# Kernel optimization log

Measured on AMD Instinct MI355X. Metric: run time of the kernel, lower is better.

The kernel has to match this reference:

```python
import jax, jax.numpy as jnp
import numpy as np

N, E, B, D, H, L = 50000, 800000, 16, 64, 128, 2


def _lin(h, w, b):
    return h @ w + b


def _scatter_mean(v, idx, n):
    s = jax.ops.segment_sum(v, idx, num_segments=n)
    c = jax.ops.segment_sum(jnp.ones((v.shape[0],), v.dtype), idx, num_segments=n)
    return s / jnp.maximum(c, 1.0)[:, None]


def setup_inputs() -> dict:
    key = jax.random.key(0)
    ks = iter(jax.random.split(key, 40))

    def p(*shape):
        return jax.random.normal(next(ks), shape, dtype=jnp.float32) * 0.05

    inp = {
        "x": jax.random.normal(next(ks), (N, D), dtype=jnp.float32),
        "edge_attr": jax.random.normal(next(ks), (E, D), dtype=jnp.float32),
        "u": jax.random.normal(next(ks), (B, D), dtype=jnp.float32),
        "e_w1": p(L, 4 * D, H), "e_b1": p(L, H),
        "e_w2": p(L, H, H), "e_b2": p(L, H),
        "e_w3": p(L, H, D), "e_b3": p(L, D),
        "n1_w1": p(L, 2 * D, H), "n1_b1": p(L, H),
        "n1_w2": p(L, H, H), "n1_b2": p(L, H),
        "n2_w1": p(L, D + H + D, H), "n2_b1": p(L, H),
        "n2_w2": p(L, H, D), "n2_b2": p(L, D),
        "g_w1": p(L, 3 * D, H), "g_b1": p(L, H),
        "g_w2": p(L, H, D), "g_b2": p(L, D),
        "edge_index": jax.random.randint(next(ks), (2, E), 0, N, dtype=jnp.int32),
        "batch": jnp.sort(jax.random.randint(next(ks), (N,), 0, B, dtype=jnp.int32)),
    }
    return inp


def _forward(x, edge_attr, u, params, edge_index, batch):
    row, col = edge_index[0], edge_index[1]
    eb = batch[row]  # [E] graph id per edge
    x0, e0, u0 = x, edge_attr, u
    for l in range(L):
        (e_w1, e_b1, e_w2, e_b2, e_w3, e_b3,
         n1_w1, n1_b1, n1_w2, n1_b2,
         n2_w1, n2_b1, n2_w2, n2_b2,
         g_w1, g_b1, g_w2, g_b2) = [pm[l] for pm in params]
        # Edge model: [E, e+2n+u] -> MLP -> [E, D]
        h = jnp.concatenate([x[row], x[col], edge_attr, u[eb]], axis=1)
        h = jax.nn.relu(_lin(h, e_w1, e_b1))
        h = jax.nn.relu(_lin(h, e_w2, e_b2))
        edge_attr = _lin(h, e_w3, e_b3)
        # Node model: gather src node + edge, MLP1, scatter_mean onto dest, MLP2
        se = jnp.concatenate([x[row], edge_attr], axis=1)  # [E, 2D]
        se = _lin(jax.nn.relu(_lin(se, n1_w1, n1_b1)), n1_w2, n1_b2)
        agg = _scatter_mean(se, col, N)  # [N, H]
        xh = jnp.concatenate([x, agg, u[batch]], axis=1)
        x = _lin(jax.nn.relu(_lin(xh, n2_w1, n2_b1)), n2_w2, n2_b2)
        # Global model: per-graph means of updated nodes/edges
        e_agg = _scatter_mean(edge_attr, eb, B)
        n_agg = _scatter_mean(x, batch, B)
        uh = jnp.concatenate([u, n_agg, e_agg], axis=1)
        u = _lin(jax.nn.relu(_lin(uh, g_w1, g_b1)), g_w2, g_b2)
    return x + x0, edge_attr + e0, u + u0


def reference(x, edge_attr, u, e_w1, e_b1, e_w2, e_b2, e_w3, e_b3, n1_w1, n1_b1, n1_w2, n1_b2, n2_w1, n2_b1, n2_w2, n2_b2, g_w1, g_b1, g_w2, g_b2, edge_index, batch):
    params = (e_w1, e_b1, e_w2, e_b2, e_w3, e_b3,
              n1_w1, n1_b1, n1_w2, n1_b2,
              n2_w1, n2_b1, n2_w2, n2_b2,
              g_w1, g_b1, g_w2, g_b2)
    return _forward(x, edge_attr, u, params, edge_index, batch)
```

## Files before the change

### kernel.cpp

```cpp
#include <hip/hip_runtime.h>

#define N_NODES 50000
#define E_EDGES 800000
#define NG 16
#define DD 64
#define HH 128
#define NB_SCAN 49
#define EREP 32

typedef __attribute__((ext_vector_type(8))) __bf16 bf16x8;
typedef __attribute__((ext_vector_type(4))) float f32x4;
typedef unsigned int uint;
typedef unsigned short ushort;
typedef __attribute__((ext_vector_type(4))) uint uint4v;

#define MFMA16(a,b,c) __builtin_amdgcn_mfma_f32_16x16x32_bf16((a),(b),(c),0,0,0)

__device__ __forceinline__ ushort f2bf(float f){
  uint u = __builtin_bit_cast(uint, f);
  u += 0x7fffu + ((u >> 16) & 1u);
  return (ushort)(u >> 16);
}
__device__ __forceinline__ uint pk2(float a, float b){
  return (uint)f2bf(a) | ((uint)f2bf(b) << 16);
}
__device__ __forceinline__ float bflo(uint u){ return __builtin_bit_cast(float, u << 16); }
__device__ __forceinline__ float bfhi(uint u){ return __builtin_bit_cast(float, u & 0xffff0000u); }

__device__ __forceinline__ void bar(){
  asm volatile("s_waitcnt lgkmcnt(0)" ::: "memory");
  __builtin_amdgcn_s_barrier();
}
#define VMWAIT(n) asm volatile("s_waitcnt vmcnt(" #n ")" ::: "memory")

__device__ __forceinline__ void gload16(const void* g, void* l){
  __builtin_amdgcn_global_load_lds(
      (const __attribute__((address_space(1))) unsigned int*)g,
      (__attribute__((address_space(3))) unsigned int*)l, 16, 0, 0);
}

__device__ __forceinline__ bf16x8 ldfrag(const char* base, int row, int byteoff){
  uint4v v = *(const uint4v*)(base + row*256 + (byteoff ^ ((row & 7) << 4)));
  return __builtin_bit_cast(bf16x8, v);
}
__device__ __forceinline__ uint4v ld_chunk(const char* base, int row, int c16){
  return *(const uint4v*)(base + row*256 + ((c16*16) ^ ((row & 7) << 4)));
}
__device__ __forceinline__ void st_h(char* base, int row, int col, float v){
  *(ushort*)(base + row*256 + ((col*2) ^ ((row & 7) << 4))) = f2bf(v);
}
__device__ __forceinline__ void st_chunk(char* base, int row, int c16, uint4v v){
  *(uint4v*)(base + row*256 + ((c16*16) ^ ((row & 7) << 4))) = v;
}
__device__ __forceinline__ bf16x8 ldfrag128(const char* base, int row, int byteoff){
  uint4v v = *(const uint4v*)(base + row*128 + (byteoff ^ ((row & 7) << 4)));
  return __builtin_bit_cast(bf16x8, v);
}
__device__ __forceinline__ void st_chunk128(char* base, int row, int c16, uint4v v){
  *(uint4v*)(base + row*128 + ((c16*16) ^ ((row & 7) << 4))) = v;
}
__device__ __forceinline__ void pack16_128(char* dst, int r, int c16, const float* src){
  float4 lo = *(const float4*)src;
  float4 hi = *(const float4*)(src + 4);
  uint4v v; v.x = pk2(lo.x, lo.y); v.y = pk2(lo.z, lo.w);
  v.z = pk2(hi.x, hi.y); v.w = pk2(hi.z, hi.w);
  st_chunk128(dst, r, c16, v);
}

__device__ __forceinline__ void stage_b(char* sB, const ushort* wt,
                                        int Nout, int Ktot, int koff, int t, int stride){
  for (int task = t; task < Nout*16; task += stride){
    int n = task >> 4, c = task & 15;
    uint4v v = *(const uint4v*)(wt + (long)n*Ktot + koff + c*8);
    st_chunk(sB, n, c, v);
  }
}
template<int NT>
__device__ __forceinline__ void gemm_acc(const char* A, const char* B,
                                         int wv, int l15, int lhi, f32x4* acc){
  #pragma unroll
  for (int kt = 0; kt < 4; ++kt){
    bf16x8 a = ldfrag(A, wv*16 + l15, kt*64 + lhi*16);
    #pragma unroll
    for (int n = 0; n < NT; ++n){
      bf16x8 bb = ldfrag(B, n*16 + l15, kt*64 + lhi*16);
      acc[n] = MFMA16(a, bb, acc[n]);
    }
  }
}
template<int NT, bool RELU>
__device__ __forceinline__ void epi_lds(char* dst, const f32x4* acc, const float* bias,
                                        int wv, int l15, int lhi){
  #pragma unroll
  for (int n = 0; n < NT; ++n){
    float bv = bias[n*16 + l15];
    #pragma unroll
    for (int j = 0; j < 4; ++j){
      int r = wv*16 + lhi*4 + j;
      float v = acc[n][j] + bv;
      if (RELU) v = fmaxf(v, 0.f);
      st_h(dst, r, n*16 + l15, v);
    }
  }
}

__global__ void convert_x(const float* __restrict__ x, ushort* __restrict__ xbf){
  int i = blockIdx.x*256 + threadIdx.x;
  if (i < (N_NODES*DD)/8){
    float4 lo = *(const float4*)(x + (long)i*8);
    float4 hi = *(const float4*)(x + (long)i*8 + 4);
    uint4v v; v.x = pk2(lo.x, lo.y); v.y = pk2(lo.z, lo.w);
    v.z = pk2(hi.x, hi.y); v.w = pk2(hi.z, hi.w);
    *(uint4v*)(xbf + (long)i*8) = v;
  }
}

__global__ void pack_weights(const float* __restrict__ e1, const float* __restrict__ e2,
                             const float* __restrict__ e3, const float* __restrict__ n12,
                             const float* __restrict__ n21, const float* __restrict__ n22,
                             ushort* __restrict__ out){
  int idx = blockIdx.x * 256 + threadIdx.x;
  int l = idx / 114688, r = idx % 114688;
  const float* src; int K, N, off;
  if      (r <  32768){ src = e1;  K = 256; N = 128; off = 0; }
  else if (r <  49152){ src = e2;  K = 128; N = 128; off = 32768; }
  else if (r <  57344){ src = e3;  K = 128; N = 64;  off = 49152; }
  else if (r <  73728){ src = n12; K = 128; N = 128; off = 57344; }
  else if (r < 106496){ src = n21; K = 256; N = 128; off = 73728; }
  else                { src = n22; K = 128; N = 64;  off = 106496; }
  int q = r - off; int k = q / N; int n = q % N;
  out[(long)l*139264 + off + n*K + k] = f2bf(src[(long)l*K*N + q]);
}

__global__ void make_wc(const float* __restrict__ n1w1, const float* __restrict__ ew3,
                        const float* __restrict__ n1b1, const float* __restrict__ eb3,
                        ushort* __restrict__ packed, float* __restrict__ biasc){
  int l = blockIdx.x, t = threadIdx.x;
  const float* W1 = n1w1 + (long)l*128*128;
  const float* W3 = ew3 + (long)l*128*64;
  ushort* wc = packed + (long)l*139264 + 114688;
  for (int i = t; i < 8192; i += 256){
    int k = i >> 7, n = i & 127;
    wc[n*192 + k] = f2bf(W1[k*128 + n]);
  }
  for (int i = t; i < 16384; i += 256){
    int k2 = i >> 7, n = i & 127;
    float s = 0.f;
    for (int m = 0; m < 64; ++m) s += W3[k2*64 + m] * W1[(64 + m)*128 + n];
    wc[n*192 + 64 + k2] = f2bf(s);
  }
  if (t < 128){
    float s = n1b1[l*128 + t];
    for (int m = 0; m < 64; ++m) s += eb3[l*64 + m] * W1[(64 + m)*128 + t];
    biasc[l*128 + t] = s;
  }
}

__global__ void hist_kernel(const int* __restrict__ edge_index, const int* __restrict__ batch,
                            int* __restrict__ deg, float* __restrict__ cnt_eb){
  __shared__ float h[NG];
  int t = threadIdx.x;
  if (t < NG) h[t] = 0.f;
  __syncthreads();
  int e = blockIdx.x * 256 + t;
  if (e < E_EDGES){
    atomicAdd(deg + edge_index[E_EDGES + e], 1);
    atomicAdd(&h[batch[edge_index[e]]], 1.f);
  }
  __syncthreads();
  if (t < NG) atomicAdd(cnt_eb + t, h[t]);
}
__global__ void count_nodes_kernel(const int* __restrict__ batch, float* __restrict__ cnt_b){
  __shared__ float h[NG];
  int t = threadIdx.x;
  if (t < NG) h[t] = 0.f;
  __syncthreads();
  int n = blockIdx.x * 256 + t;
  if (n < N_NODES) atomicAdd(&h[batch[n]], 1.f);
  __syncthreads();
  if (t < NG) atomicAdd(cnt_b + t, h[t]);
}
__global__ void scan_a(const int* __restrict__ deg, int* __restrict__ bsum){
  __shared__ int red[1024];
  int i = blockIdx.x*1024 + threadIdx.x;
  red[threadIdx.x] = (i < N_NODES) ? deg[i] : 0;
  __syncthreads();
  for (int s = 512; s > 0; s >>= 1){
    if ((int)threadIdx.x < s) red[threadIdx.x] += red[threadIdx.x + s];
    __syncthreads();
  }
  if (threadIdx.x == 0) bsum[blockIdx.x] = red[0];
}
__global__ void scan_b(const int* __restrict__ bsum, int* __restrict__ bbase){
  if (threadIdx.x == 0){
    int run = 0;
    for (int b = 0; b < NB_SCAN; ++b){ int v = bsum[b]; bbase[b] = run; run += v; }
  }
}
__global__ void scan_c(const int* __restrict__ deg, const int* __restrict__ bbase,
                       int* __restrict__ off, int* __restrict__ cursor){
  __shared__ int sc[1024];
  int i = blockIdx.x*1024 + threadIdx.x;
  int v = (i < N_NODES) ? deg[i] : 0;
  sc[threadIdx.x] = v;
  __syncthreads();
  for (int d = 1; d < 1024; d <<= 1){
    int add = ((int)threadIdx.x >= d) ? sc[threadIdx.x - d] : 0;
    __syncthreads();
    sc[threadIdx.x] += add;
    __syncthreads();
  }
  if (i < N_NODES){
    int ex = sc[threadIdx.x] - v + bbase[blockIdx.x];
    off[i] = ex; cursor[i] = ex;
  }
}
__global__ void fill_kernel(const int* __restrict__ edge_index, int* __restrict__ cursor,
                            int* __restrict__ pos){
  int e = blockIdx.x*256 + threadIdx.x;
  if (e < E_EDGES){
    int c = edge_index[E_EDGES + e];
    pos[e] = atomicAdd(&cursor[c], 1);
  }
}

__global__ __launch_bounds__(256, 3) void k123_kernel(
    const ushort* __restrict__ xbf, const float* e_cur,
    const float* __restrict__ u_cur,
    const int* __restrict__ ei, const int* __restrict__ batch,
    const ushort* __restrict__ w1t, const ushort* __restrict__ w2t,
    const float* __restrict__ be1, const float* __restrict__ be2,
    ushort* h2g)
{
  __shared__ __align__(16) char lds[49152];
  __shared__ int sRow[128], sCol[128], sEb[128];
  char* A  = lds;
  char* B  = lds + 16384;
  char* OV = lds + 16384;
  const int t = threadIdx.x;
  const int wv = t >> 6, l15 = t & 15, lhi = (t >> 4) & 3;
  const int ebase = blockIdx.x * 128;

  if (t < 128){
    int r = ei[ebase + t];
    sRow[t] = r; sCol[t] = ei[E_EDGES + ebase + t]; sEb[t] = batch[r];
  }
  __syncthreads();

  f32x4 acc[2][8];
  #pragma unroll
  for (int m = 0; m < 2; ++m)
    #pragma unroll
    for (int n = 0; n < 8; ++n) acc[m][n] = f32x4{0,0,0,0};

  for (int c = 0; c < 4; ++c){
    #pragma unroll
    for (int it = 0; it < 4; ++it){
      int task = t + it*256, r = task >> 3, c16 = task & 7;
      if (c == 0)
        st_chunk128(A, r, c16, *(const uint4v*)(xbf + (long)sRow[r]*DD + c16*8));
      else if (c == 1)
        st_chunk128(A, r, c16, *(const uint4v*)(xbf + (long)sCol[r]*DD + c16*8));
      else if (c == 2)
        pack16_128(A, r, c16, e_cur + (long)(ebase + r)*DD + c16*8);
      else
        pack16_128(A, r, c16, u_cur + (long)sEb[r]*DD + c16*8);
    }
    #pragma unroll
    for (int it = 0; it < 4; ++it){
      int task = t + it*256, n = task >> 3, c16 = task & 7;
      st_chunk128(B, n, c16, *(const uint4v*)(w1t + (long)n*256 + c*64 + c16*8));
    }
    __syncthreads();
    #pragma unroll
    for (int kt = 0; kt < 2; ++kt){
      bf16x8 a0 = ldfrag128(A, wv*32 + l15,      kt*64 + lhi*16);
      bf16x8 a1 = ldfrag128(A, wv*32 + 16 + l15, kt*64 + lhi*16);
      #pragma unroll
      for (int n = 0; n < 8; ++n){
        bf16x8 bb = ldfrag128(B, n*16 + l15, kt*64 + lhi*16);
        acc[0][n] = MFMA16(a0, bb, acc[0][n]);
        acc[1][n] = MFMA16(a1, bb, acc[1][n]);
      }
    }
    __syncthreads();
  }
  #pragma unroll
  for (int m = 0; m < 2; ++m)
    #pragma unroll
    for (int n = 0; n < 8; ++n){
      int col = n*16 + l15;
      float bv = be1[col];
      #pragma unroll
      for (int j = 0; j < 4; ++j)
        st_h(OV, wv*32 + m*16 + lhi*4 + j, col, fmaxf(acc[m][n][j] + bv, 0.f));
    }
  __syncthreads();

  #pragma unroll
  for (int m = 0; m < 2; ++m)
    #pragma unroll
    for (int n = 0; n < 8; ++n) acc[m][n] = f32x4{0,0,0,0};
  for (int kc = 0; kc < 2; ++kc){
    #pragma unroll
    for (int it = 0; it < 4; ++it){
      int task = t + it*256, n = task >> 3, c16 = task & 7;
      st_chunk128(A, n, c16, *(const uint4v*)(w2t + (long)n*128 + kc*64 + c16*8));
    }
    __syncthreads();
    #pragma unroll
    for (int kt = 0; kt < 2; ++kt){
      bf16x8 a0 = ldfrag(OV, wv*32 + l15,      kc*128 + kt*64 + lhi*16);
      bf16x8 a1 = ldfrag(OV, wv*32 + 16 + l15, kc*128 + kt*64 + lhi*16);
      #pragma unroll
      for (int n = 0; n < 8; ++n){
        bf16x8 bb = ldfrag128(A, n*16 + l15, kt*64 + lhi*16);
        acc[0][n] = MFMA16(a0, bb, acc[0][n]);
        acc[1][n] = MFMA16(a1, bb, acc[1][n]);
      }
    }
    __syncthreads();
  }
  #pragma unroll
  for (int m = 0; m < 2; ++m)
    #pragma unroll
    for (int n = 0; n < 8; ++n){
      int col = n*16 + l15;
      float bv = be2[col];
      #pragma unroll
      for (int j = 0; j < 4; ++j)
        st_h(OV, wv*32 + m*16 + lhi*4 + j, col, fmaxf(acc[m][n][j] + bv, 0.f));
    }
  __syncthreads();
  #pragma unroll
  for (int it = 0; it < 8; ++it){
    int task = t + it*256, r = task >> 4, c16 = task & 15;
    *(uint4v*)(h2g + (long)(ebase + r)*HH + c16*8) = ld_chunk(OV, r, c16);
  }
}

template<bool CSR>
__global__ __launch_bounds__(256, 2) void k45_kernel(
    const ushort* __restrict__ xbf, const ushort* h2g,
    const int* __restrict__ ei, const int* __restrict__ batch,
    const int* __restrict__ pos_arr,
    const ushort* __restrict__ w3t, const ushort* __restrict__ wct,
    const ushort* __restrict__ w5t,
    const float* __restrict__ be3, const float* __restrict__ biasc,
    const float* __restrict__ bn12,
    float* e_outf, const float* __restrict__ e_resid,
    ushort* __restrict__ se_buf, float* __restrict__ agg_sum,
    float* __restrict__ e_agg_rep, int has_resid)
{
  __shared__ __align__(16) char lds[49152];
  __shared__ float sEagg[NG*DD];
  __shared__ int sRow[128];
  __shared__ int sDst[128];
  char* S0 = lds;
  char* S1 = lds + 16384;
  char* S2 = lds + 32768;
  char* OV = lds;
  const int t = threadIdx.x;
  const int wv = t >> 6, lane = t & 63, l15 = t & 15, lhi = (t >> 4) & 3;
  const int ebase = blockIdx.x * 128;

  auto GL = [&](const ushort* base, long stride, int koff, char* slot){
    #pragma unroll
    for (int it = 0; it < 4; ++it){
      int q = (wv*4 + it)*64 + lane;
      int r = q >> 3, cp = q & 7;
      gload16(base + (long)r*stride + koff + ((cp ^ (r & 7))*8),
              slot + (wv*4 + it)*1024);
    }
  };

  if (t < 128){
    int r = ei[ebase + t];
    sDst[t] = CSR ? pos_arr[ebase + t] : ei[E_EDGES + ebase + t];
    sRow[t] = r | (batch[r] << 16);
  }
  GL(wct, 192, 0, S1);
  GL(h2g + (long)ebase*HH, HH, 0, S2);
  bf16x8 b3[4][4];
  #pragma unroll
  for (int n = 0; n < 4; ++n)
    #pragma unroll
    for (int kk = 0; kk < 4; ++kk)
      b3[n][kk] = *(const bf16x8*)(w3t + (long)(n*16 + l15)*128 + kk*32 + lhi*8);
  for (int i = t; i < NG*DD; i += 256) sEagg[i] = 0.f;
  __syncthreads();

  #pragma unroll
  for (int it = 0; it < 4; ++it){
    int task = t + it*256, r = task >> 3, c16 = task & 7;
    st_chunk128(S0, r, c16,
        *(const uint4v*)(xbf + (long)(sRow[r] & 0xffff)*DD + c16*8));
  }
  __syncthreads();

  f32x4 acc4[2][8], acc3[2][4];
  #pragma unroll
  for (int m = 0; m < 2; ++m){
    #pragma unroll
    for (int n = 0; n < 8; ++n) acc4[m][n] = f32x4{0,0,0,0};
    #pragma unroll
    for (int n = 0; n < 4; ++n) acc3[m][n] = f32x4{0,0,0,0};
  }
  auto MM = [&](const char* A, const char* B){
    #pragma unroll
    for (int kt = 0; kt < 2; ++kt){
      bf16x8 a0 = ldfrag128(A, wv*32 + l15,      kt*64 + lhi*16);
      bf16x8 a1 = ldfrag128(A, wv*32 + 16 + l15, kt*64 + lhi*16);
      #pragma unroll
      for (int n = 0; n < 8; ++n){
        bf16x8 bb = ldfrag128(B, n*16 + l15, kt*64 + lhi*16);
        acc4[0][n] = MFMA16(a0, bb, acc4[0][n]);
        acc4[1][n] = MFMA16(a1, bb, acc4[1][n]);
      }
    }
  };
  auto MM3 = [&](const char* A, const char* B, int kkbase){
    #pragma unroll
    for (int kt = 0; kt < 2; ++kt){
      bf16x8 a0 = ldfrag128(A, wv*32 + l15,      kt*64 + lhi*16);
      bf16x8 a1 = ldfrag128(A, wv*32 + 16 + l15, kt*64 + lhi*16);
      #pragma unroll
      for (int n = 0; n < 8; ++n){
        bf16x8 bb = ldfrag128(B, n*16 + l15, kt*64 + lhi*16);
        acc4[0][n] = MFMA16(a0, bb, acc4[0][n]);
        acc4[1][n] = MFMA16(a1, bb, acc4[1][n]);
      }
      #pragma unroll
      for (int n = 0; n < 4; ++n){
        acc3[0][n] = MFMA16(a0, b3[n][kkbase + kt], acc3[0][n]);
        acc3[1][n] = MFMA16(a1, b3[n][kkbase + kt], acc3[1][n]);
      }
    }
  };

  MM(S0, S1);
  bar();
  GL(wct, 192, 64, S1);
  GL(h2g + (long)ebase*HH, HH, 64, S0);
  VMWAIT(4);
  __builtin_amdgcn_s_barrier();
  MM3(S2, S1, 0);
  bar();
  GL(wct, 192, 128, S1);
  GL(w5t, 128, 0, S2);
  VMWAIT(4);
  __builtin_amdgcn_s_barrier();
  MM3(S0, S1, 2);
  bar();
  #pragma unroll
  for (int m = 0; m < 2; ++m)
    #pragma unroll
    for (int n = 0; n < 8; ++n){
      int col = n*16 + l15;
      float bv = biasc[col];
      #pragma unroll
      for (int j = 0; j < 4; ++j)
        st_h(OV, wv*32 + m*16 + lhi*4 + j, col, fmaxf(acc4[m][n][j] + bv, 0.f));
    }
  VMWAIT(0);
  bar();
  f32x4 acc5[2][8];
  #pragma unroll
  for (int m = 0; m < 2; ++m)
    #pragma unroll
    for (int n = 0; n < 8; ++n) acc5[m][n] = f32x4{0,0,0,0};
  #pragma unroll
  for (int kt = 0; kt < 2; ++kt){
    bf16x8 a0 = ldfrag(OV, wv*32 + l15,      kt*64 + lhi*16);
    bf16x8 a1 = ldfrag(OV, wv*32 + 16 + l15, kt*64 + lhi*16);
    #pragma unroll
    for (int n = 0; n < 8; ++n){
      bf16x8 bb = ldfrag128(S2, n*16 + l15, kt*64 + lhi*16);
      acc5[0][n] = MFMA16(a0, bb, acc5[0][n]);
      acc5[1][n] = MFMA16(a1, bb, acc5[1][n]);
    }
  }
  bar();
  GL(w5t, 128, 64, S2);
  VMWAIT(0);
  __builtin_amdgcn_s_barrier();
  #pragma unroll
  for (int kt = 0; kt < 2; ++kt){
    bf16x8 a0 = ldfrag(OV, wv*32 + l15,      128 + kt*64 + lhi*16);
    bf16x8 a1 = ldfrag(OV, wv*32 + 16 + l15, 128 + kt*64 + lhi*16);
    #pragma unroll
    for (int n = 0; n < 8; ++n){
      bf16x8 bb = ldfrag128(S2, n*16 + l15, kt*64 + lhi*16);
      acc5[0][n] = MFMA16(a0, bb, acc5[0][n]);
      acc5[1][n] = MFMA16(a1, bb, acc5[1][n]);
    }
  }
  bar();

  if (CSR){
    #pragma unroll
    for (int m = 0; m < 2; ++m)
      #pragma unroll
      for (int n = 0; n < 8; ++n){
        int col = n*16 + l15;
        float bv = bn12[col];
        #pragma unroll
        for (int j = 0; j < 4; ++j)
          st_h(OV, wv*32 + m*16 + lhi*4 + j, col, acc5[m][n][j] + bv);
      }
    bar();
    #pragma unroll
    for (int it = 0; it < 8; ++it){
      int task = t + it*256, r = task >> 4, c16 = task & 15;
      *(uint4v*)(se_buf + (long)sDst[r]*HH + c16*8) = ld_chunk(OV, r, c16);
    }
  } else {
    #pragma unroll
    for (int m = 0; m < 2; ++m)
      #pragma unroll
      for (int n = 0; n < 8; ++n){
        int col = n*16 + l15;
        float bv = bn12[col];
        #pragma unroll
        for (int j = 0; j < 4; ++j){
          int row = wv*32 + m*16 + lhi*4 + j;
          atomicAdd(agg_sum + (long)sDst[row]*HH + col, acc5[m][n][j] + bv);
        }
      }
  }
  #pragma unroll
  for (int m = 0; m < 2; ++m)
    #pragma unroll
    for (int n = 0; n < 4; ++n){
      int col = n*16 + l15;
      float bv = be3[col];
      #pragma unroll
      for (int j = 0; j < 4; ++j){
        int row = wv*32 + m*16 + lhi*4 + j;
        float v = acc3[m][n][j] + bv;
        long eg = (long)(ebase + row)*DD + col;
        e_outf[eg] = has_resid ? (v + e_resid[eg]) : v;
        atomicAdd(&sEagg[(sRow[row] >> 16)*DD + col], v);
      }
    }
  __syncthreads();
  float* dst = e_agg_rep + (long)(blockIdx.x & (EREP - 1))*NG*DD;
  for (int i = t; i < NG*DD; i += 256) atomicAdd(dst + i, sEagg[i]);
}

template<bool CSR>
__global__ __launch_bounds__(256, 2) void node_kernel(
    const float* __restrict__ x_cur, const float* __restrict__ u_cur,
    const float* __restrict__ x_resid, const int* __restrict__ batch,
    const ushort* __restrict__ se_buf, const int* __restrict__ deg,
    const int* __restrict__ off, const float* __restrict__ agg_sum,
    const ushort* __restrict__ w_n21, const ushort* __restrict__ w_n22,
    const float* __restrict__ b_n21, const float* __restrict__ b_n22,
    float* __restrict__ x_out, float* __restrict__ n_agg, int has_resid)
{
  __shared__ __align__(16) char sA[16384];
  __shared__ __align__(16) char sB[32768];
  __shared__ __align__(16) char sH[16384];
  __shared__ int sBat[64], sDeg[64], sOff[64];
  __shared__ float sRinv[64];
  __shared__ float sNagg[NG*DD];

  const int t = threadIdx.x;
  const int wv = t >> 6, ln = t & 63, l15 = ln & 15, lhi = ln >> 4;
  const int n0 = blockIdx.x * 64;

  if (t < 64){
    int nd = n0 + t;
    int ok = nd < N_NODES;
    sBat[t] = ok ? batch[nd] : 0;
    int d = ok ? deg[nd] : 0;
    sDeg[t] = d;
    sOff[t] = ok ? off[nd] : 0;
    sRinv[t] = 1.f / fmaxf((float)d, 1.f);
  }
  for (int i = t; i < NG*DD; i += 256) sNagg[i] = 0.f;
  __syncthreads();

  float s[32];
  const int r4 = t >> 2, q = t & 3;
  if (CSR){
    #pragma unroll
    for (int k = 0; k < 32; ++k) s[k] = 0.f;
    int d = sDeg[r4], o = sOff[r4];
    for (int i = 0; i < d; ++i){
      const ushort* src = se_buf + (long)(o + i)*HH + q*32;
      #pragma unroll
      for (int c = 0; c < 4; ++c){
        uint4v v = *(const uint4v*)(src + c*8);
        #pragma unroll
        for (int jj = 0; jj < 4; ++jj){
          s[c*8 + jj*2]     += bflo(v[jj]);
          s[c*8 + jj*2 + 1] += bfhi(v[jj]);
        }
      }
    }
    float riv = sRinv[r4];
    #pragma unroll
    for (int k = 0; k < 32; ++k) s[k] *= riv;
  }

  f32x4 acc[8];
  #pragma unroll
  for (int n = 0; n < 8; ++n) acc[n] = f32x4{0.f,0.f,0.f,0.f};

  for (int half = 0; half < 2; ++half){
    if (CSR){
      for (int task = t; task < 512; task += 256){
        int r = task >> 3, c = task & 7;
        int nd = n0 + r;
        bool ok = nd < N_NODES;
        float4 lo = {0,0,0,0}, hi = {0,0,0,0};
        if (ok){
          const float* src = (half == 0) ? (x_cur + (long)nd*DD + c*8)
                                         : (u_cur + (long)sBat[r]*DD + c*8);
          lo = *(const float4*)src; hi = *(const float4*)(src + 4);
        }
        uint4v v; v.x = pk2(lo.x, lo.y); v.y = pk2(lo.z, lo.w);
        v.z = pk2(hi.x, hi.y); v.w = pk2(hi.z, hi.w);
        st_chunk(sA, r, (half == 0) ? c : (8 + c), v);
      }
      if ((half == 0 && q < 2) || (half == 1 && q >= 2)){
        int cbase = (half == 0) ? (8 + q*4) : ((q - 2)*4);
        #pragma unroll
        for (int cc = 0; cc < 4; ++cc){
          uint4v v;
          v.x = pk2(s[cc*8+0], s[cc*8+1]); v.y = pk2(s[cc*8+2], s[cc*8+3]);
          v.z = pk2(s[cc*8+4], s[cc*8+5]); v.w = pk2(s[cc*8+6], s[cc*8+7]);
          st_chunk(sA, r4, cbase + cc, v);
        }
      }
    } else {
      for (int task = t; task < 1024; task += 256){
        int r = task >> 4, c = task & 15;
        int nd = n0 + r;
        bool ok = nd < N_NODES;
        float scale = 1.f;
        const float* src;
        if (half == 0){
          if (c < 8) src = x_cur + (long)nd*DD + c*8;
          else { src = agg_sum + (long)nd*HH + (c-8)*8; scale = sRinv[r]; }
        } else {
          if (c < 8){ src = agg_sum + (long)nd*HH + 64 + c*8; scale = sRinv[r]; }
          else src = u_cur + (long)sBat[r]*DD + (c-8)*8;
        }
        float4 lo = {0,0,0,0}, hi = {0,0,0,0};
        if (ok){ lo = *(const float4*)src; hi = *(const float4*)(src + 4); }
        uint4v v; v.x = pk2(lo.x*scale, lo.y*scale); v.y = pk2(lo.z*scale, lo.w*scale);
        v.z = pk2(hi.x*scale, hi.y*scale); v.w = pk2(hi.z*scale, hi.w*scale);
        st_chunk(sA, r, c, v);
      }
    }
    stage_b(sB, w_n21, 128, 256, half*128, t, 256);
    __syncthreads();
    gemm_acc<8>(sA, sB, wv, l15, lhi, acc);
    __syncthreads();
  }
  epi_lds<8, true>(sH, acc, b_n21, wv, l15, lhi);
  stage_b(sB, w_n22, 64, 128, 0, t, 256);
  __syncthreads();

  f32x4 acc2[4];
  #pragma unroll
  for (int n = 0; n < 4; ++n) acc2[n] = f32x4{0.f,0.f,0.f,0.f};
  gemm_acc<4>(sH, sB, wv, l15, lhi, acc2);

  #pragma unroll
  for (int n = 0; n < 4; ++n){
    float bv = b_n22[n*16 + l15];
    #pragma unroll
    for (int j = 0; j < 4; ++j){
      int r = wv*16 + lhi*4 + j;
      int nd = n0 + r;
      if (nd < N_NODES){
        int col = n*16 + l15;
        float v = acc2[n][j] + bv;
        long xg = (long)nd*DD + col;
        x_out[xg] = has_resid ? (v + x_resid[xg]) : v;
        atomicAdd(&sNagg[sBat[r]*DD + col], v);
      }
    }
  }
  __syncthreads();
  for (int i = t; i < NG*DD; i += 256) atomicAdd(n_agg + i, sNagg[i]);
}

__global__ void global_kernel(const float* __restrict__ u_cur, const float* __restrict__ n_agg,
                              const float* __restrict__ e_agg_rep, const float* __restrict__ cnt_b,
                              const float* __restrict__ cnt_e,
                              const float* __restrict__ g_w1, const float* __restrict__ g_b1,
                              const float* __restrict__ g_w2, const float* __restrict__ g_b2,
                              const float* __restrict__ u_resid, float* __restrict__ u_out,
                              int has_resid)
{
  int g = blockIdx.x, t = threadIdx.x;
  __shared__ float uh[192];
  __shared__ float hb[128];
  float v;
  if (t < 64)       v = u_cur[g*64 + t];
  else if (t < 128) v = n_agg[g*64 + (t-64)] / fmaxf(cnt_b[g], 1.f);
  else {
    float s = 0.f;
    for (int c = 0; c < EREP; ++c) s += e_agg_rep[c*NG*DD + g*64 + (t-128)];
    v = s / fmaxf(cnt_e[g], 1.f);
  }
  uh[t] = v;
  __syncthreads();
  if (t < 128){
    float s = g_b1[t];
    for (int k = 0; k < 192; ++k) s += uh[k] * g_w1[k*128 + t];
    hb[t] = fmaxf(s, 0.f);
  }
  __syncthreads();
  if (t < 64){
    float s = g_b2[t];
    for (int k = 0; k < 128; ++k) s += hb[k] * g_w2[k*64 + t];
    if (has_resid) s += u_resid[g*64 + t];
    u_out[g*64 + t] = s;
  }
}

extern "C" void kernel_launch(void* const* d_in, const int* in_sizes, int n_in,
                              void* d_out, int out_size, void* d_ws, size_t ws_size,
                              hipStream_t stream)
{
  const float* x0   = (const float*)d_in[0];
  const float* e0   = (const float*)d_in[1];
  const float* u0   = (const float*)d_in[2];
  const float* e_w1 = (const float*)d_in[3];
  const float* e_b1 = (const float*)d_in[4];
  const float* e_w2 = (const float*)d_in[5];
  const float* e_b2 = (const float*)d_in[6];
  const float* e_w3 = (const float*)d_in[7];
  const float* e_b3 = (const float*)d_in[8];
  const float* n1_w1 = (const float*)d_in[9];
  const float* n1_b1 = (const float*)d_in[10];
  const float* n1_w2 = (const float*)d_in[11];
  const float* n1_b2 = (const float*)d_in[12];
  const float* n2_w1 = (const float*)d_in[13];
  const float* n2_b1 = (const float*)d_in[14];
  const float* n2_w2 = (const float*)d_in[15];
  const float* n2_b2 = (const float*)d_in[16];
  const float* g_w1 = (const float*)d_in[17];
  const float* g_b1 = (const float*)d_in[18];
  const float* g_w2 = (const float*)d_in[19];
  const float* g_b2 = (const float*)d_in[20];
  const int* edge_index = (const int*)d_in[21];
  const int* batch      = (const int*)d_in[22];

  float* out_x = (float*)d_out;
  float* out_e = out_x + (long)N_NODES*DD;
  float* out_u = out_e + (long)E_EDGES*DD;

  char* ws = (char*)d_ws;
  int*   deg    = (int*)(ws + 0);
  int*   off    = (int*)(ws + 200000);
  int*   cursor = (int*)(ws + 400000);
  int*   bsum   = (int*)(ws + 600000);
  int*   bbase  = (int*)(ws + 600256);
  float* cnt_eb = (float*)(ws + 600512);
  float* cnt_b  = (float*)(ws + 600576);
  float* n_agg  = (float*)(ws + 604736);
  float* biascf = (float*)(ws + 608832);
  ushort* packed = (ushort*)(ws + 609856);
  float* e_agg_rep = (float*)(ws + 1166912);
  ushort* xbf = (ushort*)(ws + 1297984);
  const size_t big = 7697984;
  bool use_csr = ws_size >= (size_t)(big + 204800000 + 3200000);
  ushort* se_buf = (ushort*)(ws + big);
  int*    pos    = (int*)(ws + big + 204800000);
  float*  agg_sum = (float*)(ws + big);

  (void)hipMemsetAsync(deg, 0, 200000, stream);
  (void)hipMemsetAsync(cnt_eb, 0, 128, stream);
  pack_weights<<<896, 256, 0, stream>>>(e_w1, e_w2, e_w3, n1_w2, n2_w1, n2_w2, packed);
  make_wc<<<2, 256, 0, stream>>>(n1_w1, e_w3, n1_b1, e_b3, packed, biascf);
  hist_kernel<<<3125, 256, 0, stream>>>(edge_index, batch, deg, cnt_eb);
  count_nodes_kernel<<<196, 256, 0, stream>>>(batch, cnt_b);
  if (use_csr){
    scan_a<<<NB_SCAN, 1024, 0, stream>>>(deg, bsum);
    scan_b<<<1, 64, 0, stream>>>(bsum, bbase);
    scan_c<<<NB_SCAN, 1024, 0, stream>>>(deg, bbase, off, cursor);
    fill_kernel<<<3125, 256, 0, stream>>>(edge_index, cursor, pos);
  }

  const float* xc = x0;
  const float* ec = e0;
  const float* uc = u0;
  for (int l = 0; l < 2; ++l){
    (void)hipMemsetAsync(n_agg, 0, 4096, stream);
    (void)hipMemsetAsync(e_agg_rep, 0, EREP*NG*DD*4, stream);
    if (!use_csr)
      (void)hipMemsetAsync(agg_sum, 0, (size_t)N_NODES*HH*4, stream);
    convert_x<<<1563, 256, 0, stream>>>(xc, xbf);
    const ushort* P = packed + (long)l*139264;
    k123_kernel<<<6250, 256, 0, stream>>>(
        xbf, ec, uc, edge_index, batch,
        P + 0, P + 32768, e_b1 + l*128, e_b2 + l*128,
        (ushort*)out_e);
    if (use_csr){
      k45_kernel<true><<<6250, 256, 0, stream>>>(
          xbf, (const ushort*)out_e, edge_index, batch, pos,
          P + 49152, P + 114688, P + 57344,
          e_b3 + l*64, biascf + l*128, n1_b2 + l*128,
          out_e, e0, se_buf, agg_sum, e_agg_rep, l == 1);
      node_kernel<true><<<782, 256, 0, stream>>>(
          xc, uc, x0, batch, se_buf, deg, off, agg_sum,
          P + 73728, P + 106496, n2_b1 + l*128, n2_b2 + l*64,
          out_x, n_agg, l == 1);
    } else {
      k45_kernel<false><<<6250, 256, 0, stream>>>(
          xbf, (const ushort*)out_e, edge_index, batch, pos,
          P + 49152, P + 114688, P + 57344,
          e_b3 + l*64, biascf + l*128, n1_b2 + l*128,
          out_e, e0, se_buf, agg_sum, e_agg_rep, l == 1);
      node_kernel<false><<<782, 256, 0, stream>>>(
          xc, uc, x0, batch, se_buf, deg, off, agg_sum,
          P + 73728, P + 106496, n2_b1 + l*128, n2_b2 + l*64,
          out_x, n_agg, l == 1);
    }
    global_kernel<<<NG, 192, 0, stream>>>(
        uc, n_agg, e_agg_rep, cnt_b, cnt_eb,
        g_w1 + l*192*128, g_b1 + l*128, g_w2 + l*128*64, g_b2 + l*64,
        u0, out_u, l == 1);
    xc = out_x; ec = out_e; uc = out_u;
  }
}
```

Before: 1.758 ms.

## Emit bf16 edge and node features from producers to skip conversions in layer 2

In layer 1, the edge kernel now writes the updated edge features as bf16 into the h2g/out_e buffer instead of fp32. Layer 2's edge MLP kernel then loads them directly without packing. The node kernel also writes a bf16 copy of x, so the per-layer convert_x launch is dropped in the CSR path. This cuts fp32 write/read traffic and one kernel launch, but it aliases the out_e buffer as bf16 storage between layers and relies on that buffer not being needed as fp32 until layer 2 overwrites it.

```diff
diff --git a/kernel.cpp b/kernel.cpp
--- a/kernel.cpp
+++ b/kernel.cpp
@@ -56,8 +56,14 @@
   uint4v v = *(const uint4v*)(base + row*128 + (byteoff ^ ((row & 7) << 4)));
   return __builtin_bit_cast(bf16x8, v);
 }
+__device__ __forceinline__ uint4v ld_chunk128(const char* base, int row, int c16){
+  return *(const uint4v*)(base + row*128 + ((c16*16) ^ ((row & 7) << 4)));
+}
 __device__ __forceinline__ void st_chunk128(char* base, int row, int c16, uint4v v){
   *(uint4v*)(base + row*128 + ((c16*16) ^ ((row & 7) << 4))) = v;
+}
+__device__ __forceinline__ void st_h128(char* base, int row, int col, float v){
+  *(ushort*)(base + row*128 + ((col*2) ^ ((row & 7) << 4))) = f2bf(v);
 }
 __device__ __forceinline__ void pack16_128(char* dst, int r, int c16, const float* src){
   float4 lo = *(const float4*)src;
@@ -224,6 +230,7 @@
   }
 }
 
+template<bool EBF>
 __global__ __launch_bounds__(256, 3) void k123_kernel(
     const ushort* __restrict__ xbf, const float* e_cur,
     const float* __restrict__ u_cur,
@@ -261,9 +268,12 @@
         st_chunk128(A, r, c16, *(const uint4v*)(xbf + (long)sRow[r]*DD + c16*8));
       else if (c == 1)
         st_chunk128(A, r, c16, *(const uint4v*)(xbf + (long)sCol[r]*DD + c16*8));
-      else if (c == 2)
-        pack16_128(A, r, c16, e_cur + (long)(ebase + r)*DD + c16*8);
-      else
+      else if (c == 2){
+        if (EBF)
+          st_chunk128(A, r, c16, *(const uint4v*)(h2g + (long)(ebase + r)*HH + c16*8));
+        else
+          pack16_128(A, r, c16, e_cur + (long)(ebase + r)*DD + c16*8);
+      } else
         pack16_128(A, r, c16, u_cur + (long)sEb[r]*DD + c16*8);
     }
     #pragma unroll
@@ -508,11 +518,51 @@
         for (int j = 0; j < 4; ++j)
           st_h(OV, wv*32 + m*16 + lhi*4 + j, col, acc5[m][n][j] + bv);
       }
+    if (!has_resid){
+      #pragma unroll
+      for (int m = 0; m < 2; ++m)
+        #pragma unroll
+        for (int n = 0; n < 4; ++n){
+          int col = n*16 + l15;
+          float bv = be3[col];
+          #pragma unroll
+          for (int j = 0; j < 4; ++j){
+            int row = wv*32 + m*16 + lhi*4 + j;
+            float v = acc3[m][n][j] + bv;
+            st_h128(S2, row, col, v);
+            atomicAdd(&sEagg[(sRow[row] >> 16)*DD + col], v);
+          }
+        }
+    }
     bar();
     #pragma unroll
     for (int it = 0; it < 8; ++it){
       int task = t + it*256, r = task >> 4, c16 = task & 15;
       *(uint4v*)(se_buf + (long)sDst[r]*HH + c16*8) = ld_chunk(OV, r, c16);
+    }
+    if (!has_resid){
+      ushort* ebf = (ushort*)e_outf;
+      #pragma unroll
+      for (int it = 0; it < 4; ++it){
+        int task = t + it*256, r = task >> 3, c16 = task & 7;
+        *(uint4v*)(ebf + (long)(ebase + r)*HH + c16*8) = ld_chunk128(S2, r, c16);
+      }
+    } else {
+      #pragma unroll
+      for (int m = 0; m < 2; ++m)
+        #pragma unroll
+        for (int n = 0; n < 4; ++n){
+          int col = n*16 + l15;
+          float bv = be3[col];
+          #pragma unroll
+          for (int j = 0; j < 4; ++j){
+            int row = wv*32 + m*16 + lhi*4 + j;
+            float v = acc3[m][n][j] + bv;
+            long eg = (long)(ebase + row)*DD + col;
+            e_outf[eg] = v + e_resid[eg];
+            atomicAdd(&sEagg[(sRow[row] >> 16)*DD + col], v);
+          }
+        }
     }
   } else {
     #pragma unroll
@@ -527,22 +577,22 @@
           atomicAdd(agg_sum + (long)sDst[row]*HH + col, acc5[m][n][j] + bv);
         }
       }
-  }
-  #pragma unroll
-  for (int m = 0; m < 2; ++m)
-    #pragma unroll
-    for (int n = 0; n < 4; ++n){
-      int col = n*16 + l15;
-      float bv = be3[col];
-      #pragma unroll
-      for (int j = 0; j < 4; ++j){
-        int row = wv*32 + m*16 + lhi*4 + j;
-        float v = acc3[m][n][j] + bv;
-        long eg = (long)(ebase + row)*DD + col;
-        e_outf[eg] = has_resid ? (v + e_resid[eg]) : v;
-        atomicAdd(&sEagg[(sRow[row] >> 16)*DD + col], v);
-      }
-    }
+    #pragma unroll
+    for (int m = 0; m < 2; ++m)
+      #pragma unroll
+      for (int n = 0; n < 4; ++n){
+        int col = n*16 + l15;
+        float bv = be3[col];
+        #pragma unroll
+        for (int j = 0; j < 4; ++j){
+          int row = wv*32 + m*16 + lhi*4 + j;
+          float v = acc3[m][n][j] + bv;
+          long eg = (long)(ebase + row)*DD + col;
+          e_outf[eg] = has_resid ? (v + e_resid[eg]) : v;
+          atomicAdd(&sEagg[(sRow[row] >> 16)*DD + col], v);
+        }
+      }
+  }
   __syncthreads();
   float* dst = e_agg_rep + (long)(blockIdx.x & (EREP - 1))*NG*DD;
   for (int i = t; i < NG*DD; i += 256) atomicAdd(dst + i, sEagg[i]);
@@ -556,7 +606,8 @@
     const int* __restrict__ off, const float* __restrict__ agg_sum,
     const ushort* __restrict__ w_n21, const ushort* __restrict__ w_n22,
     const float* __restrict__ b_n21, const float* __restrict__ b_n22,
-    float* __restrict__ x_out, float* __restrict__ n_agg, int has_resid)
+    float* __restrict__ x_out, ushort* __restrict__ xbf_out,
+    float* __restrict__ n_agg, int has_resid)
 {
   __shared__ __align__(16) char sA[16384];
   __shared__ __align__(16) char sB[32768];
@@ -680,7 +731,9 @@
         int col = n*16 + l15;
         float v = acc2[n][j] + bv;
         long xg = (long)nd*DD + col;
-        x_out[xg] = has_resid ? (v + x_resid[xg]) : v;
+        float vw = has_resid ? (v + x_resid[xg]) : v;
+        x_out[xg] = vw;
+        if (!has_resid) xbf_out[xg] = f2bf(vw);
         atomicAdd(&sNagg[sBat[r]*DD + col], v);
       }
     }
@@ -781,6 +834,7 @@
   make_wc<<<2, 256, 0, stream>>>(n1_w1, e_w3, n1_b1, e_b3, packed, biascf);
   hist_kernel<<<3125, 256, 0, stream>>>(edge_index, batch, deg, cnt_eb);
   count_nodes_kernel<<<196, 256, 0, stream>>>(batch, cnt_b);
+  convert_x<<<1563, 256, 0, stream>>>(x0, xbf);
   if (use_csr){
     scan_a<<<NB_SCAN, 1024, 0, stream>>>(deg, bsum);
     scan_b<<<1, 64, 0, stream>>>(bsum, bbase);
@@ -794,14 +848,21 @@
   for (int l = 0; l < 2; ++l){
     (void)hipMemsetAsync(n_agg, 0, 4096, stream);
     (void)hipMemsetAsync(e_agg_rep, 0, EREP*NG*DD*4, stream);
-    if (!use_csr)
+    if (!use_csr){
       (void)hipMemsetAsync(agg_sum, 0, (size_t)N_NODES*HH*4, stream);
-    convert_x<<<1563, 256, 0, stream>>>(xc, xbf);
+      if (l == 1) convert_x<<<1563, 256, 0, stream>>>(xc, xbf);
+    }
     const ushort* P = packed + (long)l*139264;
-    k123_kernel<<<6250, 256, 0, stream>>>(
-        xbf, ec, uc, edge_index, batch,
-        P + 0, P + 32768, e_b1 + l*128, e_b2 + l*128,
-        (ushort*)out_e);
+    if (use_csr && l == 1)
+      k123_kernel<true><<<6250, 256, 0, stream>>>(
+          xbf, ec, uc, edge_index, batch,
+          P + 0, P + 32768, e_b1 + l*128, e_b2 + l*128,
+          (ushort*)out_e);
+    else
+      k123_kernel<false><<<6250, 256, 0, stream>>>(
+          xbf, ec, uc, edge_index, batch,
+          P + 0, P + 32768, e_b1 + l*128, e_b2 + l*128,
+          (ushort*)out_e);
     if (use_csr){
       k45_kernel<true><<<6250, 256, 0, stream>>>(
           xbf, (const ushort*)out_e, edge_index, batch, pos,
@@ -811,7 +872,7 @@
       node_kernel<true><<<782, 256, 0, stream>>>(
           xc, uc, x0, batch, se_buf, deg, off, agg_sum,
           P + 73728, P + 106496, n2_b1 + l*128, n2_b2 + l*64,
-          out_x, n_agg, l == 1);
+          out_x, xbf, n_agg, l == 1);
     } else {
       k45_kernel<false><<<6250, 256, 0, stream>>>(
           xbf, (const ushort*)out_e, edge_index, batch, pos,
@@ -821,7 +882,7 @@
       node_kernel<false><<<782, 256, 0, stream>>>(
           xc, uc, x0, batch, se_buf, deg, off, agg_sum,
           P + 73728, P + 106496, n2_b1 + l*128, n2_b2 + l*64,
-          out_x, n_agg, l == 1);
+          out_x, xbf, n_agg, l == 1);
     }
     global_kernel<<<NG, 192, 0, stream>>>(
         uc, n_agg, e_agg_rep, cnt_b, cnt_eb,
```

Result: faster. 1.709 ms (-2.8%).
